# Kernel tuning notes

Hardware: AMD Instinct MI355X
Metric: run time of the kernel (lower is better)

## Reference

```python
import jax, jax.numpy as jnp
import numpy as np

EPS = 1e-6          # VN leaky-relu denominator eps (vn_layers.py)
NEG_SLOPE = 0.2     # VNLinearLeakyReLU default negative_slope
K = 3               # pointops.interpolation default k
DIST_EPS = 1e-8     # interpolation inverse-distance eps


def vn_linear_leakyrelu(x, w_feat, w_dir):
    # x: [B, Cin, 3, N]; w_*: [Cout, Cin]  (bias-free Linears over channel dim)
    p = jnp.einsum('oc,bcvn->bovn', w_feat, x)
    d = jnp.einsum('oc,bcvn->bovn', w_dir, x)
    dot = jnp.sum(p * d, axis=2, keepdims=True)          # [B,Cout,1,N]
    d2 = jnp.sum(d * d, axis=2, keepdims=True)
    mask = (dot >= 0).astype(x.dtype)
    proj = p - (dot / (d2 + EPS)) * d                    # reflect negative part onto plane perp to d
    return NEG_SLOPE * p + (1.0 - NEG_SLOPE) * (mask * p + (1.0 - mask) * proj)


def interpolation(p2, p1, feat, b, n2, n1):
    # p2: [b*n2,3] coarse coords, p1: [b*n1,3] fine coords, feat: [C,3,b*n2]
    # k-NN inverse-squared-distance interpolation, segment-local per cloud.
    C = feat.shape[0]
    p2b = p2.reshape(b, n2, 3)
    p1b = p1.reshape(b, n1, 3)
    featb = feat.reshape(C * 3, b, n2).transpose(1, 2, 0)  # [b, n2, C*3]

    def per_batch(q, s, f):
        d2 = jnp.sum((q[:, None, :] - s[None, :, :]) ** 2, axis=-1)  # [n1,n2]
        neg_d2, idx = jax.lax.top_k(-d2, K)                          # k smallest sq-dists
        w = 1.0 / (-neg_d2 + DIST_EPS)
        w = w / jnp.sum(w, axis=1, keepdims=True)                    # [n1,K]
        return jnp.einsum('nk,nkc->nc', w, f[idx])                   # [n1, C*3]

    out = jax.vmap(per_batch)(p1b, p2b, featb)                       # [b, n1, C*3]
    return out.reshape(b, n1, C, 3).transpose(2, 3, 0, 1).reshape(C, 3, b * n1)


def setup_inputs() -> dict:
    key = jax.random.key(0)
    ks = jax.random.split(key, 8)
    b, n1, n2 = 4, 16384, 4096
    in_planes, out_planes = 128, 64
    p1 = jax.random.uniform(ks[0], (b * n1, 3), dtype=jnp.float32)
    p2 = jax.random.uniform(ks[1], (b * n2, 3), dtype=jnp.float32)
    x1 = jax.random.normal(ks[2], (1, out_planes, 3, b * n1), dtype=jnp.float32)
    x2 = jax.random.normal(ks[3], (1, in_planes, 3, b * n2), dtype=jnp.float32)
    o1 = (jnp.arange(1, b + 1, dtype=jnp.int32)) * n1   # cumulative offsets
    o2 = (jnp.arange(1, b + 1, dtype=jnp.int32)) * n2
    s1 = 1.0 / np.sqrt(out_planes)
    s2 = 1.0 / np.sqrt(in_planes)
    w1_feat = jax.random.uniform(ks[4], (out_planes, out_planes), jnp.float32, -s1, s1)
    w1_dir = jax.random.uniform(ks[5], (out_planes, out_planes), jnp.float32, -s1, s1)
    w2_feat = jax.random.uniform(ks[6], (out_planes, in_planes), jnp.float32, -s2, s2)
    w2_dir = jax.random.uniform(ks[7], (out_planes, in_planes), jnp.float32, -s2, s2)
    return {"p1": p1, "x1": x1, "o1": o1, "p2": p2, "x2": x2, "o2": o2,
            "w1_feat": w1_feat, "w1_dir": w1_dir, "w2_feat": w2_feat, "w2_dir": w2_dir}


def reference(p1, x1, o1, p2, x2, o2, w1_feat, w1_dir, w2_feat, w2_dir):
    b = o1.shape[0]
    n1 = x1.shape[-1] // b
    n2 = x2.shape[-1] // b
    y1 = vn_linear_leakyrelu(x1, w1_feat, w1_dir)            # [1,Cout,3,N1]
    y2 = vn_linear_leakyrelu(x2, w2_feat, w2_dir)[0]         # squeeze(0) -> [Cout,3,N2]
    up = interpolation(p2, p1, y2, b, n2, n1)                # [Cout,3,N1]
    return y1 + up
```

## Files before the change

### kernel.cpp

```cpp
#include <hip/hip_runtime.h>

#define N1T 65536
#define N2T 16384
#define COUT 64
#define CH 192
#define GRD 8
#define HCELL 0.125f

typedef unsigned short bhalf;
typedef __attribute__((ext_vector_type(8))) short short8;
typedef __attribute__((ext_vector_type(4))) float f32x4;

__device__ __forceinline__ bhalf f2bf(float f) {
    unsigned u = __float_as_uint(f);
    return (bhalf)((u + 0x7FFFu + ((u >> 16) & 1u)) >> 16);
}
__device__ __forceinline__ float bf2f(bhalf h) {
    return __uint_as_float(((unsigned)h) << 16);
}

__global__ __launch_bounds__(256) void wconv_kernel(
    const float* __restrict__ w1f, const float* __restrict__ w1d,
    const float* __restrict__ w2f, const float* __restrict__ w2d,
    bhalf* __restrict__ o1fh, bhalf* __restrict__ o1fl,
    bhalf* __restrict__ o1dh, bhalf* __restrict__ o1dl,
    bhalf* __restrict__ o2fh, bhalf* __restrict__ o2fl,
    bhalf* __restrict__ o2dh, bhalf* __restrict__ o2dl) {
    const int i = blockIdx.x * 256 + threadIdx.x;
    if (i < 4096) {
        const float a = w1f[i]; const bhalf ah = f2bf(a);
        o1fh[i] = ah; o1fl[i] = f2bf(a - bf2f(ah));
        const float b = w1d[i]; const bhalf bh = f2bf(b);
        o1dh[i] = bh; o1dl[i] = f2bf(b - bf2f(bh));
    }
    const float a = w2f[i]; const bhalf ah = f2bf(a);
    o2fh[i] = ah; o2fl[i] = f2bf(a - bf2f(ah));
    const float b = w2d[i]; const bhalf bh = f2bf(b);
    o2dh[i] = bh; o2dl[i] = f2bf(b - bf2f(bh));
}

template<int CIN, int N, bool CM, int NT>
__global__ __launch_bounds__(512) void vn_mfma_kernel(
    const float* __restrict__ x,
    const bhalf* __restrict__ wfh, const bhalf* __restrict__ wfl,
    const bhalf* __restrict__ wdh, const bhalf* __restrict__ wdl,
    const int*   __restrict__ idxs,
    const float* __restrict__ wts,
    const float* __restrict__ y2t,
    float* __restrict__ out)
{
    constexpr int ROWS = CIN * 3;
    constexpr int LDSC = CIN * 3 + 8;
    constexpr int NB   = (NT > 1) ? 2 : 1;
    constexpr int NLD  = ROWS * 8 / 512;
    __shared__ __align__(16) bhalf xs_h[NB][32][LDSC];
    __shared__ __align__(16) bhalf xs_l[NB][32][LDSC];

    const int tid  = threadIdx.x;
    const int lane = tid & 63;
    const int wave = tid >> 6;
    const int r16  = lane & 15;
    const int hh   = lane >> 4;
    const int ot   = wave & 3;
    const int sW   = wave >> 2;
    const int pt   = sW * 16 + r16;
    const int tile0 = blockIdx.x * NT;
    const int chb  = ot * 48 + hh * 12;

    int gk[NT][3]; float gw[NT][3];
    if constexpr (CM) {
#pragma unroll
        for (int t = 0; t < NT; ++t) {
            const int n = (tile0 + t) * 32 + pt;
#pragma unroll
            for (int r = 0; r < 3; ++r) {
                gk[t][r] = idxs[r * N1T + n];
                gw[t][r] = wts[r * N1T + n];
            }
        }
    }

    const int wofs = (ot * 16 + r16) * CIN + hh * 8;
    const bhalf* __restrict__ pfh = wfh + wofs;
    const bhalf* __restrict__ pfl = wfl + wofs;
    const bhalf* __restrict__ pdh = wdh + wofs;
    const bhalf* __restrict__ pdl = wdl + wofs;
    const int hs = ((hh ^ (r16 >> 2)) & 3) * 8;

    auto LOADT = [&](float4 (&st)[NLD], int t) {
#pragma unroll
        for (int r = 0; r < NLD; ++r) {
            const int i4 = r * 512 + tid;
            const int row = i4 >> 3, p4 = i4 & 7;
            st[r] = *(const float4*)&x[(size_t)row * N + (size_t)(tile0 + t) * 32 + p4 * 4];
        }
    };
    auto WRITET = [&](const float4 (&st)[NLD], int b) {
#pragma unroll
        for (int r = 0; r < NLD; ++r) {
            const int i4 = r * 512 + tid;
            const int row = i4 >> 3, p4 = i4 & 7;
            const int c = row / 3, vv = row - c * 3;
            const int colS = (vv * CIN + c) ^ ((p4 & 3) << 3);
            const float vals[4] = {st[r].x, st[r].y, st[r].z, st[r].w};
#pragma unroll
            for (int j = 0; j < 4; ++j) {
                const bhalf h = f2bf(vals[j]);
                xs_h[b][p4*4+j][colS] = h;
                xs_l[b][p4*4+j][colS] = f2bf(vals[j] - bf2f(h));
            }
        }
    };
    auto GATHER_ISSUE = [&](float4 (&g0)[3], float4 (&g1)[3], float4 (&g2)[3], int t) {
        const float* __restrict__ r0 = y2t + (size_t)gk[t][0] * CH + chb;
        const float* __restrict__ r1 = y2t + (size_t)gk[t][1] * CH + chb;
        const float* __restrict__ r2 = y2t + (size_t)gk[t][2] * CH + chb;
#pragma unroll
        for (int q = 0; q < 3; ++q) {
            g0[q] = *(const float4*)&r0[q * 4];
            g1[q] = *(const float4*)&r1[q * 4];
            g2[q] = *(const float4*)&r2[q * 4];
        }
    };
    auto MFMA_VN = [&](float (&rr)[12], int b) {
        const f32x4 zero = {0.f, 0.f, 0.f, 0.f};
        f32x4 accP[3], accD[3];
#pragma unroll
        for (int v = 0; v < 3; ++v) { accP[v] = zero; accD[v] = zero; }
#pragma unroll
        for (int k = 0; k < CIN / 32; ++k) {
            const short8 afh = *(const short8*)(pfh + k * 32);
            const short8 afl = *(const short8*)(pfl + k * 32);
            const short8 adh = *(const short8*)(pdh + k * 32);
            const short8 adl = *(const short8*)(pdl + k * 32);
#pragma unroll
            for (int v = 0; v < 3; ++v) {
                const short8 bh = *(const short8*)&xs_h[b][pt][v * CIN + k * 32 + hs];
                const short8 bl = *(const short8*)&xs_l[b][pt][v * CIN + k * 32 + hs];
                accP[v] = __builtin_amdgcn_mfma_f32_16x16x32_bf16(afh, bh, accP[v], 0, 0, 0);
                accP[v] = __builtin_amdgcn_mfma_f32_16x16x32_bf16(afl, bh, accP[v], 0, 0, 0);
                accP[v] = __builtin_amdgcn_mfma_f32_16x16x32_bf16(afh, bl, accP[v], 0, 0, 0);
                accD[v] = __builtin_amdgcn_mfma_f32_16x16x32_bf16(adh, bh, accD[v], 0, 0, 0);
                accD[v] = __builtin_amdgcn_mfma_f32_16x16x32_bf16(adl, bh, accD[v], 0, 0, 0);
                accD[v] = __builtin_amdgcn_mfma_f32_16x16x32_bf16(adh, bl, accD[v], 0, 0, 0);
            }
        }
#pragma unroll
        for (int reg = 0; reg < 4; ++reg) {
            const float p0 = accP[0][reg], p1 = accP[1][reg], p2 = accP[2][reg];
            const float q0 = accD[0][reg], q1 = accD[1][reg], q2 = accD[2][reg];
            const float dot = p0*q0 + p1*q1 + p2*q2;
            const float dd  = q0*q0 + q1*q1 + q2*q2;
            const float coef = (dot < 0.f) ? (0.8f * dot / (dd + 1e-6f)) : 0.f;
            rr[reg*3+0] = p0 - coef * q0;
            rr[reg*3+1] = p1 - coef * q1;
            rr[reg*3+2] = p2 - coef * q2;
        }
    };
    auto STORE_CM = [&](const float (&rr)[12],
                        const float4 (&g0)[3], const float4 (&g1)[3],
                        const float4 (&g2)[3], int t) {
        const int n = (tile0 + t) * 32 + pt;
        const float w0 = gw[t][0], w1 = gw[t][1], w2 = gw[t][2];
#pragma unroll
        for (int q = 0; q < 3; ++q) {
            const float u0 = w0*g0[q].x + w1*g1[q].x + w2*g2[q].x;
            const float u1 = w0*g0[q].y + w1*g1[q].y + w2*g2[q].y;
            const float u2 = w0*g0[q].z + w1*g1[q].z + w2*g2[q].z;
            const float u3 = w0*g0[q].w + w1*g1[q].w + w2*g2[q].w;
            out[(size_t)(chb + q*4 + 0) * N + n] = rr[q*4+0] + u0;
            out[(size_t)(chb + q*4 + 1) * N + n] = rr[q*4+1] + u1;
            out[(size_t)(chb + q*4 + 2) * N + n] = rr[q*4+2] + u2;
            out[(size_t)(chb + q*4 + 3) * N + n] = rr[q*4+3] + u3;
        }
    };
    auto STORE_PM = [&](const float (&rr)[12], int t) {
        const int n = (tile0 + t) * 32 + pt;
        float* op = out + (size_t)n * CH + chb;
        *(float4*)&op[0] = make_float4(rr[0], rr[1], rr[2],  rr[3]);
        *(float4*)&op[4] = make_float4(rr[4], rr[5], rr[6],  rr[7]);
        *(float4*)&op[8] = make_float4(rr[8], rr[9], rr[10], rr[11]);
    };

    float4 stA[NLD], stB[NLD];
    float4 gA0[3], gA1[3], gA2[3];
    float rr0[12], rr1[12];

    LOADT(stA, 0);
    WRITET(stA, 0);
    if constexpr (NT == 2) {
        LOADT(stB, 1);
        if constexpr (CM) GATHER_ISSUE(gA0, gA1, gA2, 0);
        __syncthreads();
        MFMA_VN(rr0, 0);
        WRITET(stB, 1);
        if constexpr (CM) {
            STORE_CM(rr0, gA0, gA1, gA2, 0);
            GATHER_ISSUE(gA0, gA1, gA2, 1);
        } else {
            STORE_PM(rr0, 0);
        }
        __syncthreads();
        MFMA_VN(rr1, 1);
        if constexpr (CM) STORE_CM(rr1, gA0, gA1, gA2, 1);
        else              STORE_PM(rr1, 1);
    } else {
        if constexpr (CM) GATHER_ISSUE(gA0, gA1, gA2, 0);
        __syncthreads();
        MFMA_VN(rr0, 0);
        if constexpr (CM) STORE_CM(rr0, gA0, gA1, gA2, 0);
        else              STORE_PM(rr0, 0);
    }
}

#define KNN_INSERT(d2, j)                                        \
    {                                                            \
        const bool c0 = (d2) < b0;                               \
        const bool c1 = (d2) < b1;                               \
        const bool c2 = (d2) < b2v;                              \
        const float nb2 = c2 ? (c1 ? b1 : (d2)) : b2v;           \
        const int   ni2 = c2 ? (c1 ? i1 : (j))  : i2;            \
        const float nb1 = c1 ? (c0 ? b0 : (d2)) : b1;            \
        const int   ni1 = c1 ? (c0 ? i0 : (j))  : i1;            \
        b0 = c0 ? (d2) : b0;  i0 = c0 ? (j) : i0;                \
        b1 = nb1; i1 = ni1; b2v = nb2; i2 = ni2;                 \
    }

__global__ __launch_bounds__(256) void zero_kernel(int* __restrict__ p, int n) {
    const int i = blockIdx.x * 256 + threadIdx.x;
    if (i < n) p[i] = 0;
}

__device__ __forceinline__ int cell_of(float x, float y, float z) {
    int cx = (int)(x * (float)GRD); cx = cx < 0 ? 0 : (cx > GRD-1 ? GRD-1 : cx);
    int cy = (int)(y * (float)GRD); cy = cy < 0 ? 0 : (cy > GRD-1 ? GRD-1 : cy);
    int cz = (int)(z * (float)GRD); cz = cz < 0 ? 0 : (cz > GRD-1 ? GRD-1 : cz);
    return (cz << 6) | (cy << 3) | cx;
}

__global__ __launch_bounds__(256) void bin_count_kernel(
    const float* __restrict__ p2, int* __restrict__ counts) {
    const int i = blockIdx.x * 256 + threadIdx.x;
    const float x = p2[i*3+0], y = p2[i*3+1], z = p2[i*3+2];
    const int cell = ((i >> 12) << 9) | cell_of(x, y, z);
    atomicAdd(&counts[cell], 1);
}

__global__ __launch_bounds__(256) void scan_kernel(
    const int* __restrict__ counts, int* __restrict__ off) {
    __shared__ int buf[2][256];
    const int t = threadIdx.x;
    int v[8]; int s = 0;
#pragma unroll
    for (int j = 0; j < 8; ++j) { const int tmp = counts[t*8+j]; v[j] = s; s += tmp; }
    buf[0][t] = s; __syncthreads();
    int src = 0;
    for (int d = 1; d < 256; d <<= 1) {
        int val = buf[src][t];
        if (t >= d) val += buf[src][t - d];
        buf[src ^ 1][t] = val; src ^= 1; __syncthreads();
    }
    const int incl = buf[src][t];
    const int base = incl - s;
#pragma unroll
    for (int j = 0; j < 8; ++j) off[t*8+j] = base + v[j];
    if (t == 255) off[2048] = incl;
}

__global__ __launch_bounds__(256) void bin_scatter_kernel(
    const float* __restrict__ p2, const int* __restrict__ off,
    int* __restrict__ cnt2, float4* __restrict__ binned) {
    const int i = blockIdx.x * 256 + threadIdx.x;
    const float x = p2[i*3+0], y = p2[i*3+1], z = p2[i*3+2];
    const int cell = ((i >> 12) << 9) | cell_of(x, y, z);
    const int pos = off[cell] + atomicAdd(&cnt2[cell], 1);
    binned[pos] = make_float4(x, y, z, __int_as_float(i));
}

__global__ __launch_bounds__(256) void knn_grid_kernel(
    const float* __restrict__ p1,
    const float4* __restrict__ binned,
    const int* __restrict__ off,
    int*   __restrict__ idx_out,
    float* __restrict__ w_out)
{
    const int t   = blockIdx.x * 256 + threadIdx.x;
    const int fp  = t >> 2;
    const int sub = t & 3;
    const int bi  = fp >> 14;
    const int cbase = bi << 9;

    const float qx = p1[fp*3+0], qy = p1[fp*3+1], qz = p1[fp*3+2];
    int cx = (int)(qx * (float)GRD); cx = cx < 0 ? 0 : (cx > 7 ? 7 : cx);
    int cy = (int)(qy * (float)GRD); cy = cy < 0 ? 0 : (cy > 7 ? 7 : cy);
    int cz = (int)(qz * (float)GRD); cz = cz < 0 ? 0 : (cz > 7 ? 7 : cz);

    float b0 = 1e30f, b1 = 1e30f, b2v = 1e30f;
    int   i0 = 0,     i1 = 0,     i2 = 0;

    for (int dz = -1; dz <= 1; ++dz)
    for (int dy = -1; dy <= 1; ++dy)
    for (int dx = -1; dx <= 1; ++dx) {
        const int nx = cx + dx, ny = cy + dy, nz = cz + dz;
        if ((unsigned)nx > 7u || (unsigned)ny > 7u || (unsigned)nz > 7u) continue;
        const int c = cbase + (nz << 6) + (ny << 3) + nx;
        const int s = off[c], e = off[c + 1];
        for (int k = s + sub; k < e; k += 4) {
            const float4 c4 = binned[k];
            const float ddx = qx - c4.x, ddy = qy - c4.y, ddz = qz - c4.z;
            const float d2 = fmaf(ddx, ddx, fmaf(ddy, ddy, ddz * ddz));
            const int j = __float_as_int(c4.w);
            KNN_INSERT(d2, j)
        }
    }

#pragma unroll
    for (int m = 1; m <= 2; m <<= 1) {
        const float c0v = __shfl_xor(b0, m, 4);
        const float c1v = __shfl_xor(b1, m, 4);
        const float c2v = __shfl_xor(b2v, m, 4);
        const int   j0v = __shfl_xor(i0, m, 4);
        const int   j1v = __shfl_xor(i1, m, 4);
        const int   j2v = __shfl_xor(i2, m, 4);
        KNN_INSERT(c0v, j0v)
        KNN_INSERT(c1v, j1v)
        KNN_INSERT(c2v, j2v)
    }

    float dw = 1e30f;
    if (cx >= 2) dw = fminf(dw, qx - (float)(cx - 1) * HCELL);
    if (cx <= 5) dw = fminf(dw, (float)(cx + 2) * HCELL - qx);
    if (cy >= 2) dw = fminf(dw, qy - (float)(cy - 1) * HCELL);
    if (cy <= 5) dw = fminf(dw, (float)(cy + 2) * HCELL - qy);
    if (cz >= 2) dw = fminf(dw, qz - (float)(cz - 1) * HCELL);
    if (cz <= 5) dw = fminf(dw, (float)(cz + 2) * HCELL - qz);
    const bool done = b2v < dw * dw;

    if (!done) {
        b0 = b1 = b2v = 1e30f; i0 = i1 = i2 = 0;
        const int s = bi << 12, e = (bi + 1) << 12;
        for (int k = s + sub; k < e; k += 4) {
            const float4 c4 = binned[k];
            const float ddx = qx - c4.x, ddy = qy - c4.y, ddz = qz - c4.z;
            const float d2 = fmaf(ddx, ddx, fmaf(ddy, ddy, ddz * ddz));
            const int j = __float_as_int(c4.w);
            KNN_INSERT(d2, j)
        }
#pragma unroll
        for (int m = 1; m <= 2; m <<= 1) {
            const float c0v = __shfl_xor(b0, m, 4);
            const float c1v = __shfl_xor(b1, m, 4);
            const float c2v = __shfl_xor(b2v, m, 4);
            const int   j0v = __shfl_xor(i0, m, 4);
            const int   j1v = __shfl_xor(i1, m, 4);
            const int   j2v = __shfl_xor(i2, m, 4);
            KNN_INSERT(c0v, j0v)
            KNN_INSERT(c1v, j1v)
            KNN_INSERT(c2v, j2v)
        }
    }

    if (sub == 0) {
        const float w0 = 1.f / (b0 + 1e-8f);
        const float w1 = 1.f / (b1 + 1e-8f);
        const float w2 = 1.f / (b2v + 1e-8f);
        const float inv = 1.f / (w0 + w1 + w2);
        idx_out[0*N1T + fp] = i0;
        idx_out[1*N1T + fp] = i1;
        idx_out[2*N1T + fp] = i2;
        w_out[0*N1T + fp] = w0 * inv;
        w_out[1*N1T + fp] = w1 * inv;
        w_out[2*N1T + fp] = w2 * inv;
    }
}

extern "C" void kernel_launch(void* const* d_in, const int* in_sizes, int n_in,
                              void* d_out, int out_size, void* d_ws, size_t ws_size,
                              hipStream_t stream) {
    const float* p1      = (const float*)d_in[0];
    const float* x1      = (const float*)d_in[1];
    const float* p2      = (const float*)d_in[3];
    const float* x2      = (const float*)d_in[4];
    const float* w1_feat = (const float*)d_in[6];
    const float* w1_dir  = (const float*)d_in[7];
    const float* w2_feat = (const float*)d_in[8];
    const float* w2_dir  = (const float*)d_in[9];
    float* out = (float*)d_out;

    char* ws = (char*)d_ws;
    float*  y2t    = (float*)ws;                 ws += (size_t)N2T * CH * 4;
    int*    idxs   = (int*)ws;                   ws += (size_t)3 * N1T * 4;
    float*  wts    = (float*)ws;                 ws += (size_t)3 * N1T * 4;
    int*    counts = (int*)ws;                   ws += 2048 * 4;
    int*    cnt2   = (int*)ws;                   ws += 2048 * 4;
    int*    off    = (int*)ws;                   ws += 2064 * 4;
    float4* binned = (float4*)ws;                ws += (size_t)N2T * 16;
    bhalf*  wb1fh  = (bhalf*)ws;                 ws += 4096 * 2;
    bhalf*  wb1fl  = (bhalf*)ws;                 ws += 4096 * 2;
    bhalf*  wb1dh  = (bhalf*)ws;                 ws += 4096 * 2;
    bhalf*  wb1dl  = (bhalf*)ws;                 ws += 4096 * 2;
    bhalf*  wb2fh  = (bhalf*)ws;                 ws += 8192 * 2;
    bhalf*  wb2fl  = (bhalf*)ws;                 ws += 8192 * 2;
    bhalf*  wb2dh  = (bhalf*)ws;                 ws += 8192 * 2;
    bhalf*  wb2dl  = (bhalf*)ws;                 ws += 8192 * 2;

    wconv_kernel<<<32, 256, 0, stream>>>(w1_feat, w1_dir, w2_feat, w2_dir,
                                         wb1fh, wb1fl, wb1dh, wb1dl,
                                         wb2fh, wb2fl, wb2dh, wb2dl);

    zero_kernel<<<16, 256, 0, stream>>>(counts, 4096);
    bin_count_kernel<<<N2T/256, 256, 0, stream>>>(p2, counts);
    scan_kernel<<<1, 256, 0, stream>>>(counts, off);
    bin_scatter_kernel<<<N2T/256, 256, 0, stream>>>(p2, off, cnt2, binned);
    knn_grid_kernel<<<(4*N1T)/256, 256, 0, stream>>>(p1, binned, off, idxs, wts);

    vn_mfma_kernel<128, N2T, false, 1><<<N2T/32, 512, 0, stream>>>(
        x2, wb2fh, wb2fl, wb2dh, wb2dl, nullptr, nullptr, nullptr, y2t);
    vn_mfma_kernel<64, N1T, true, 2><<<N1T/64, 512, 0, stream>>>(
        x1, wb1fh, wb1fl, wb1dh, wb1dl, idxs, wts, y2t, out);
}
```

Measured before the change: 110.9 us.

## Merge contiguous x-cells into single ranges in kNN and reorder VN tile pipeline

The kNN grid search now treats the three x-adjacent cells in each (z,y) row as one contiguous span of the binned array. That cuts the offset lookups and inner loop launches from up to 27 to up to 9, and the outer loops are unrolled. The VN MFMA kernel's two-tile schedule is also reordered: a barrier follows the first tile write, and tile 0 is computed and stored before the second tile is written to shared memory. This changes how the global loads, gathers and stores overlap with the MFMA work and shifts the barrier placement.

Measured after the change: 98.91 us. 1.12x faster.

```diff
diff --git a/kernel.cpp b/kernel.cpp
--- a/kernel.cpp
+++ b/kernel.cpp
@@ -183,32 +183,28 @@
     };
 
     float4 stA[NLD], stB[NLD];
-    float4 gA0[3], gA1[3], gA2[3];
+    float4 g0[3], g1[3], g2[3];
     float rr0[12], rr1[12];
 
     LOADT(stA, 0);
     WRITET(stA, 0);
+    __syncthreads();
     if constexpr (NT == 2) {
         LOADT(stB, 1);
-        if constexpr (CM) GATHER_ISSUE(gA0, gA1, gA2, 0);
+        if constexpr (CM) GATHER_ISSUE(g0, g1, g2, 0);
+        MFMA_VN(rr0, 0);
+        if constexpr (CM) STORE_CM(rr0, g0, g1, g2, 0);
+        else              STORE_PM(rr0, 0);
+        WRITET(stB, 1);
         __syncthreads();
-        MFMA_VN(rr0, 0);
-        WRITET(stB, 1);
-        if constexpr (CM) {
-            STORE_CM(rr0, gA0, gA1, gA2, 0);
-            GATHER_ISSUE(gA0, gA1, gA2, 1);
-        } else {
-            STORE_PM(rr0, 0);
-        }
-        __syncthreads();
+        if constexpr (CM) GATHER_ISSUE(g0, g1, g2, 1);
         MFMA_VN(rr1, 1);
-        if constexpr (CM) STORE_CM(rr1, gA0, gA1, gA2, 1);
+        if constexpr (CM) STORE_CM(rr1, g0, g1, g2, 1);
         else              STORE_PM(rr1, 1);
     } else {
-        if constexpr (CM) GATHER_ISSUE(gA0, gA1, gA2, 0);
-        __syncthreads();
+        if constexpr (CM) GATHER_ISSUE(g0, g1, g2, 0);
         MFMA_VN(rr0, 0);
-        if constexpr (CM) STORE_CM(rr0, gA0, gA1, gA2, 0);
+        if constexpr (CM) STORE_CM(rr0, g0, g1, g2, 0);
         else              STORE_PM(rr0, 0);
     }
 }
@@ -295,22 +291,29 @@
     int cy = (int)(qy * (float)GRD); cy = cy < 0 ? 0 : (cy > 7 ? 7 : cy);
     int cz = (int)(qz * (float)GRD); cz = cz < 0 ? 0 : (cz > 7 ? 7 : cz);
 
+    const int x0 = cx > 0 ? cx - 1 : 0;
+    const int x1 = cx < 7 ? cx + 1 : 7;
+
     float b0 = 1e30f, b1 = 1e30f, b2v = 1e30f;
     int   i0 = 0,     i1 = 0,     i2 = 0;
 
-    for (int dz = -1; dz <= 1; ++dz)
-    for (int dy = -1; dy <= 1; ++dy)
-    for (int dx = -1; dx <= 1; ++dx) {
-        const int nx = cx + dx, ny = cy + dy, nz = cz + dz;
-        if ((unsigned)nx > 7u || (unsigned)ny > 7u || (unsigned)nz > 7u) continue;
-        const int c = cbase + (nz << 6) + (ny << 3) + nx;
-        const int s = off[c], e = off[c + 1];
-        for (int k = s + sub; k < e; k += 4) {
-            const float4 c4 = binned[k];
-            const float ddx = qx - c4.x, ddy = qy - c4.y, ddz = qz - c4.z;
-            const float d2 = fmaf(ddx, ddx, fmaf(ddy, ddy, ddz * ddz));
-            const int j = __float_as_int(c4.w);
-            KNN_INSERT(d2, j)
+#pragma unroll
+    for (int dz = -1; dz <= 1; ++dz) {
+        const int nz = cz + dz;
+        if ((unsigned)nz > 7u) continue;
+#pragma unroll
+        for (int dy = -1; dy <= 1; ++dy) {
+            const int ny = cy + dy;
+            if ((unsigned)ny > 7u) continue;
+            const int cb = cbase + (nz << 6) + (ny << 3);
+            const int s = off[cb + x0], e = off[cb + x1 + 1];
+            for (int k = s + sub; k < e; k += 4) {
+                const float4 c4 = binned[k];
+                const float ddx = qx - c4.x, ddy = qy - c4.y, ddz = qz - c4.z;
+                const float d2 = fmaf(ddx, ddx, fmaf(ddy, ddy, ddz * ddz));
+                const int j = __float_as_int(c4.w);
+                KNN_INSERT(d2, j)
+            }
         }
     }
 
```
